# Performance work log

Hardware: AMD Instinct MI355X
Metric: run time of the kernel (lower is better)

Reference implementation:

```python
import jax, jax.numpy as jnp
import numpy as np

B, S, D = 8, 2048, 768


def setup_inputs() -> dict:
    key = jax.random.key(0)
    ks = jax.random.split(key, 16)
    def lin(kw, kb, din, dout):
        # torch nn.Linear default init: U(-1/sqrt(din), 1/sqrt(din))
        bound = 1.0 / np.sqrt(din)
        W = jax.random.uniform(kw, (din, dout), minval=-bound, maxval=bound, dtype=jnp.float32)
        b = jax.random.uniform(kb, (dout,), minval=-bound, maxval=bound, dtype=jnp.float32)
        return W, b
    Wq1, bq1 = lin(ks[0], ks[1], D, D)
    Wk1, bk1 = lin(ks[2], ks[3], D, D)
    Wv1, bv1 = lin(ks[4], ks[5], D, D)
    Wq2, bq2 = lin(ks[6], ks[7], D, D)
    Wk2, bk2 = lin(ks[8], ks[9], D, D)
    Wv2, bv2 = lin(ks[10], ks[11], D, D)
    Wf, bf = lin(ks[12], ks[13], 2 * D, D)
    self_x = jax.random.normal(ks[14], (B, S, D), dtype=jnp.float32)
    conv_x = jax.random.normal(ks[15], (B, S, D), dtype=jnp.float32)
    return {
        "self_x": self_x, "conv_x": conv_x,
        "Wq1": Wq1, "bq1": bq1, "Wk1": Wk1, "bk1": bk1, "Wv1": Wv1, "bv1": bv1,
        "Wq2": Wq2, "bq2": bq2, "Wk2": Wk2, "bk2": bk2, "Wv2": Wv2, "bv2": bv2,
        "Wf": Wf, "bf": bf,
    }


def reference(self_x, conv_x, Wq1, bq1, Wk1, bk1, Wv1, bv1,
              Wq2, bq2, Wk2, bk2, Wv2, bv2, Wf, bf):
    scale = jnp.asarray(Wk1.shape[-1] ** 0.5, dtype=self_x.dtype)

    # direction 1: queries from self_x, keys/values from conv_x
    Q1 = self_x @ Wq1 + bq1            # [B,S,D]
    K1 = conv_x @ Wk1 + bk1
    V1 = conv_x @ Wv1 + bv1
    attn1 = jnp.einsum('bqd,bkd->bqk', Q1, K1) / scale
    # NOTE: softmax over dim=1 (the QUERY axis), as in the original module
    w1 = jax.nn.softmax(attn1, axis=1)
    attn_out1 = jnp.einsum('bqk,bkd->bqd', w1, V1)

    # direction 2: queries from conv_x, keys/values from self_x
    Q2 = conv_x @ Wq2 + bq2
    K2 = self_x @ Wk2 + bk2
    V2 = self_x @ Wv2 + bv2
    attn2 = jnp.einsum('bqd,bkd->bqk', Q2, K2) / scale
    w2 = jax.nn.softmax(attn2, axis=1)
    attn_out2 = jnp.einsum('bqk,bkd->bqd', w2, V2)

    a1 = jax.nn.sigmoid(jnp.tanh(attn_out1))
    a2 = jax.nn.sigmoid(jnp.tanh(attn_out2))
    out1 = a2 * self_x + (1.0 - a2) * conv_x
    out2 = a1 * conv_x + (1.0 - a1) * self_x
    fused = jnp.concatenate([out1, out2], axis=-1)  # [B,S,2D]
    return fused @ Wf + bf
```

## Files before the change

kernel.cpp:

```cpp
#include <hip/hip_runtime.h>
#include <hip/hip_bf16.h>

#define BM 128
#define BN 128
#define BK 64

typedef short short8 __attribute__((ext_vector_type(8)));
typedef float f32x4 __attribute__((ext_vector_type(4)));

using bf = __hip_bfloat16;

static const int NOSPLIT = 1 << 30;

__device__ __forceinline__ void gld16(const void* g, void* l)
{
    __builtin_amdgcn_global_load_lds(
        (__attribute__((address_space(1))) void*)g,
        (__attribute__((address_space(3))) void*)l, 16, 0, 0);
}

__device__ __forceinline__ int lofs(int row, int kg8)
{
    return row * 64 + ((kg8 ^ (row & 7)) << 3);
}

__global__ __launch_bounds__(256)
void cast_bf16(const float* __restrict__ src, bf* __restrict__ dst, int n)
{
    int i = (blockIdx.x * 256 + threadIdx.x) * 4;
    if (i >= n) return;
    float4 v = *(const float4*)(src + i);
    bf o[4] = { __float2bfloat16(v.x), __float2bfloat16(v.y),
                __float2bfloat16(v.z), __float2bfloat16(v.w) };
    *(uint2*)(dst + i) = *(const uint2*)o;
}

__global__ __launch_bounds__(256)
void transpose_cast_w(const float* __restrict__ W, bf* __restrict__ Wt,
                      int Kd, int Nd)
{
    __shared__ float tile[32][33];
    int k0 = blockIdx.y * 32, n0 = blockIdx.x * 32;
    int t = threadIdx.x;
    int r = t >> 3, c = (t & 7) * 4;
    float4 v = *(const float4*)(W + (size_t)(k0 + r) * Nd + n0 + c);
    tile[r][c] = v.x; tile[r][c+1] = v.y; tile[r][c+2] = v.z; tile[r][c+3] = v.w;
    __syncthreads();
    bf o[4] = { __float2bfloat16(tile[c][r]),   __float2bfloat16(tile[c+1][r]),
                __float2bfloat16(tile[c+2][r]), __float2bfloat16(tile[c+3][r]) };
    *(uint2*)(Wt + (size_t)(n0 + r) * Kd + k0 + c) = *(const uint2*)o;
}

template <typename CT, bool TC>
__global__ __launch_bounds__(256)
void gemm_nt(const bf* __restrict__ A, const bf* __restrict__ A2, int splitA, int lda,
             const bf* __restrict__ Bt, int ldb,
             const float* __restrict__ bias, CT* __restrict__ C, int ldc,
             int K, long long strA, long long strB, long long strC)
{
    __shared__ __align__(16) ushort sA[2][BM * 64];
    __shared__ __align__(16) ushort sB[2][BN * 64];

    const int z = blockIdx.z;
    A  += (long long)z * strA;
    A2 += (long long)z * strA;
    Bt += (long long)z * strB;
    C  += (long long)z * strC;

    const int t = threadIdx.x;
    const int m0 = blockIdx.x * BM;
    const int n0 = blockIdx.y * BN;
    const int wave = t >> 6, lane = t & 63;
    const int wm = wave >> 1, wn = wave & 1;
    const int lcol = lane & 15, quad = lane >> 4;
    const int rl = lane >> 3, cslot = lane & 7;

    auto stage = [&](int kt, int c) {
        const bf* Asrc = (kt < splitA) ? A : A2;
        const int ktt = (kt < splitA) ? kt : kt - splitA;
        #pragma unroll
        for (int it = 0; it < 4; ++it) {
            int br  = it * 32 + wave * 8;
            int row = br + rl;
            int kg  = cslot ^ rl;
            gld16(Asrc + (size_t)(m0 + row) * lda + ktt + kg * 8, &sA[c][br * 64]);
            gld16(Bt   + (size_t)(n0 + row) * ldb + kt  + kg * 8, &sB[c][br * 64]);
        }
    };

    f32x4 acc[4][4] = {};

    stage(0, 0);
    __syncthreads();
    int cur = 0;
    for (int kt = 0; kt < K; kt += BK) {
        if (kt + BK < K) stage(kt + BK, cur ^ 1);

        #pragma unroll
        for (int h = 0; h < 2; ++h) {
            short8 af[4], bfr[4];
            #pragma unroll
            for (int i = 0; i < 4; ++i)
                af[i] = *(const short8*)&sA[cur][lofs(wm * 64 + i * 16 + lcol, h * 4 + quad)];
            #pragma unroll
            for (int j = 0; j < 4; ++j)
                bfr[j] = *(const short8*)&sB[cur][lofs(wn * 64 + j * 16 + lcol, h * 4 + quad)];
            #pragma unroll
            for (int i = 0; i < 4; ++i)
                #pragma unroll
                for (int j = 0; j < 4; ++j)
                    acc[i][j] = __builtin_amdgcn_mfma_f32_16x16x32_bf16(af[i], bfr[j], acc[i][j], 0, 0, 0);
        }
        __syncthreads();
        cur ^= 1;
    }

    #pragma unroll
    for (int j = 0; j < 4; ++j) {
        int col = n0 + wn * 64 + j * 16 + lcol;
        float bv = bias ? bias[col] : 0.0f;
        #pragma unroll
        for (int i = 0; i < 4; ++i) {
            int row = m0 + wm * 64 + i * 16 + quad * 4;
            if (!TC) {
                #pragma unroll
                for (int r4 = 0; r4 < 4; ++r4)
                    C[(size_t)(row + r4) * ldc + col] = (CT)(acc[i][j][r4] + bv);
            } else {
                bf o[4];
                #pragma unroll
                for (int r4 = 0; r4 < 4; ++r4)
                    o[r4] = __float2bfloat16(acc[i][j][r4] + bv);
                *(uint2*)((bf*)C + (size_t)col * ldc + row) = *(const uint2*)o;
            }
        }
    }
}

__global__ __launch_bounds__(256)
void scores_exp(const bf* __restrict__ Q, const bf* __restrict__ Km,
                bf* __restrict__ E, float* __restrict__ colsum,
                int Dd, float rscale)
{
    const int S = 2048;
    __shared__ __align__(16) ushort sA[2][BM * 64];
    __shared__ __align__(16) ushort sB[2][BN * 64];

    const int z = blockIdx.z;
    Q  += (size_t)z * S * Dd;
    Km += (size_t)z * S * Dd;
    E  += (size_t)z * S * S;
    colsum += (size_t)z * S;

    const int t = threadIdx.x;
    const int m0 = blockIdx.x * BM;
    const int n0 = blockIdx.y * BN;
    const int wave = t >> 6, lane = t & 63;
    const int wm = wave >> 1, wn = wave & 1;
    const int lcol = lane & 15, quad = lane >> 4;
    const int rl = lane >> 3, cslot = lane & 7;

    auto stage = [&](int kt, int c) {
        #pragma unroll
        for (int it = 0; it < 4; ++it) {
            int br  = it * 32 + wave * 8;
            int row = br + rl;
            int kg  = cslot ^ rl;
            gld16(Q  + (size_t)(m0 + row) * Dd + kt + kg * 8, &sA[c][br * 64]);
            gld16(Km + (size_t)(n0 + row) * Dd + kt + kg * 8, &sB[c][br * 64]);
        }
    };

    f32x4 acc[4][4] = {};

    stage(0, 0);
    __syncthreads();
    int cur = 0;
    for (int kt = 0; kt < Dd; kt += BK) {
        if (kt + BK < Dd) stage(kt + BK, cur ^ 1);

        #pragma unroll
        for (int h = 0; h < 2; ++h) {
            short8 af[4], bfr[4];
            #pragma unroll
            for (int i = 0; i < 4; ++i)
                af[i] = *(const short8*)&sA[cur][lofs(wm * 64 + i * 16 + lcol, h * 4 + quad)];
            #pragma unroll
            for (int j = 0; j < 4; ++j)
                bfr[j] = *(const short8*)&sB[cur][lofs(wn * 64 + j * 16 + lcol, h * 4 + quad)];
            #pragma unroll
            for (int a = 0; a < 4; ++a)
                #pragma unroll
                for (int b = 0; b < 4; ++b)
                    acc[a][b] = __builtin_amdgcn_mfma_f32_16x16x32_bf16(bfr[a], af[b], acc[a][b], 0, 0, 0);
        }
        __syncthreads();
        cur ^= 1;
    }

    #pragma unroll
    for (int a = 0; a < 4; ++a) {
        const int kk = n0 + wn * 64 + a * 16 + quad * 4;
        f32x4 csum = {0.f, 0.f, 0.f, 0.f};
        #pragma unroll
        for (int b = 0; b < 4; ++b) {
            const int q = m0 + wm * 64 + b * 16 + lcol;
            bf o[4];
            #pragma unroll
            for (int r = 0; r < 4; ++r) {
                float e = __expf(acc[a][b][r] * rscale);
                o[r] = __float2bfloat16(e);
                csum[r] += e;
            }
            *(uint2*)(E + (size_t)q * S + kk) = *(const uint2*)o;
        }
        #pragma unroll
        for (int msk = 1; msk < 16; msk <<= 1) {
            csum[0] += __shfl_xor(csum[0], msk);
            csum[1] += __shfl_xor(csum[1], msk);
            csum[2] += __shfl_xor(csum[2], msk);
            csum[3] += __shfl_xor(csum[3], msk);
        }
        if (lcol == 0) {
            atomicAdd(&colsum[kk + 0], csum[0]);
            atomicAdd(&colsum[kk + 1], csum[1]);
            atomicAdd(&colsum[kk + 2], csum[2]);
            atomicAdd(&colsum[kk + 3], csum[3]);
        }
    }
}

__global__ __launch_bounds__(256)
void scale_vt(bf* __restrict__ Vt, const float* __restrict__ cs, int ldv)
{
    int col = (blockIdx.x * 256 + threadIdx.x) * 4;
    bf* p = Vt + (size_t)blockIdx.y * ldv + col;
    bf v[4]; *(uint2*)v = *(const uint2*)p;
    float4 c4 = *(const float4*)(cs + col);
    v[0] = __float2bfloat16(__bfloat162float(v[0]) / c4.x);
    v[1] = __float2bfloat16(__bfloat162float(v[1]) / c4.y);
    v[2] = __float2bfloat16(__bfloat162float(v[2]) / c4.z);
    v[3] = __float2bfloat16(__bfloat162float(v[3]) / c4.w);
    *(uint2*)p = *(const uint2*)v;
}

__global__ __launch_bounds__(256)
void gate_fuse(const bf* __restrict__ O1, const bf* __restrict__ O2,
               const float* __restrict__ SX, const float* __restrict__ CX,
               bf* __restrict__ F1, bf* __restrict__ F2, int n)
{
    int i = (blockIdx.x * 256 + threadIdx.x) * 4;
    if (i >= n) return;
    bf o1[4], o2[4], f1[4], f2[4];
    *(uint2*)o1 = *(const uint2*)(O1 + i);
    *(uint2*)o2 = *(const uint2*)(O2 + i);
    float4 sx = *(const float4*)(SX + i);
    float4 cx = *(const float4*)(CX + i);
    #pragma unroll
    for (int e = 0; e < 4; ++e) {
        float s = (&sx.x)[e], c = (&cx.x)[e];
        float a1 = 1.0f / (1.0f + __expf(-tanhf(__bfloat162float(o1[e]))));
        float a2 = 1.0f / (1.0f + __expf(-tanhf(__bfloat162float(o2[e]))));
        f1[e] = __float2bfloat16(a2 * s + (1.0f - a2) * c);
        f2[e] = __float2bfloat16(a1 * c + (1.0f - a1) * s);
    }
    *(uint2*)(F1 + i) = *(const uint2*)f1;
    *(uint2*)(F2 + i) = *(const uint2*)f2;
}

extern "C" void kernel_launch(void* const* d_in, const int* in_sizes, int n_in,
                              void* d_out, int out_size, void* d_ws, size_t ws_size,
                              hipStream_t stream)
{
    const int B = 8, S = 2048, D = 768;
    const int M = B * S;

    const float* SX = (const float*)d_in[0];
    const float* CX = (const float*)d_in[1];
    const float* Wsrc[7] = { (const float*)d_in[2],  (const float*)d_in[4],
                             (const float*)d_in[6],  (const float*)d_in[8],
                             (const float*)d_in[10], (const float*)d_in[12],
                             (const float*)d_in[14] };
    const float* bias[7] = { (const float*)d_in[3],  (const float*)d_in[5],
                             (const float*)d_in[7],  (const float*)d_in[9],
                             (const float*)d_in[11], (const float*)d_in[13],
                             (const float*)d_in[15] };
    float* out = (float*)d_out;

    char* w = (char*)d_ws;
    const size_t MD  = (size_t)M * D * sizeof(bf);
    const size_t WSZ = (size_t)D * D * sizeof(bf);
    const size_t SSB = (size_t)S * S * sizeof(bf);
    bf* Xs = (bf*)(w);
    bf* Xc = (bf*)(w + MD);
    bf* Wt[7];
    for (int i = 0; i < 7; ++i) Wt[i] = (bf*)(w + 2 * MD + i * WSZ);
    char* base2 = w + 2 * MD + 8 * WSZ;
    bf* Q  = (bf*)(base2);
    bf* Kb = (bf*)(base2 + MD);
    bf* Vt = (bf*)(base2 + 2 * MD);
    bf* O1 = (bf*)(base2 + 3 * MD);
    float* cs = (float*)(base2 + 4 * MD);
    char* Eb0 = base2 + 4 * MD + (size_t)2 * B * S * sizeof(float);
    bf* E = (bf*)Eb0;
    int cb;
    {
        size_t fixed = (size_t)(Eb0 - w);
        size_t avail = ws_size > fixed ? ws_size - fixed : SSB;
        long long c = (long long)(avail / SSB);
        cb = c < 1 ? 1 : (c > 8 ? 8 : (int)c);
    }
    bf* O2 = Xs;
    bf* F1 = Kb;
    bf* F2 = Vt;

    (void)hipMemsetAsync(cs, 0, (size_t)2 * B * S * sizeof(float), stream);

    dim3 blk(256);
    {
        int n = M * D;
        cast_bf16<<<dim3(n / 1024), blk, 0, stream>>>(SX, Xs, n);
        cast_bf16<<<dim3(n / 1024), blk, 0, stream>>>(CX, Xc, n);
        for (int i = 0; i < 6; ++i)
            transpose_cast_w<<<dim3(D / 32, D / 32), blk, 0, stream>>>(Wsrc[i], Wt[i], D, D);
        transpose_cast_w<<<dim3(D / 32, 2 * D / 32), blk, 0, stream>>>(Wsrc[6], Wt[6], 2 * D, D);
    }

    dim3 gProj(M / BM, D / BN);
    const float rscale = 1.0f / sqrtf((float)D);
    const size_t SD = (size_t)S * D;
    const long long SS = (long long)S * S;

    for (int dir = 0; dir < 2; ++dir) {
        const bf* Xq = dir == 0 ? Xs : Xc;
        const bf* Xk = dir == 0 ? Xc : Xs;
        bf* Wq = Wt[dir * 3 + 0];
        bf* Wk = Wt[dir * 3 + 1];
        bf* Wv = Wt[dir * 3 + 2];
        const float* bq = bias[dir * 3 + 0];
        const float* bk = bias[dir * 3 + 1];
        const float* bv = bias[dir * 3 + 2];
        bf* O = dir == 0 ? O1 : O2;
        float* csd = cs + (size_t)dir * B * S;

        gemm_nt<bf, false><<<gProj, blk, 0, stream>>>(Xq, Xq, NOSPLIT, D, Wq, D, bq, Q,  D, D, 0, 0, 0);
        gemm_nt<bf, false><<<gProj, blk, 0, stream>>>(Xk, Xk, NOSPLIT, D, Wk, D, bk, Kb, D, D, 0, 0, 0);
        gemm_nt<bf, true ><<<gProj, blk, 0, stream>>>(Xk, Xk, NOSPLIT, D, Wv, D, bv, Vt, M, D, 0, 0, 0);

        for (int c0 = 0; c0 < B; c0 += cb) {
            int cbc = (B - c0 < cb) ? (B - c0) : cb;
            scores_exp<<<dim3(S / BM, S / BN, cbc), blk, 0, stream>>>(
                Q + c0 * SD, Kb + c0 * SD, E, csd + (size_t)c0 * S, D, rscale);
            scale_vt<<<dim3(cbc * S / 1024, D), blk, 0, stream>>>(
                Vt + (size_t)c0 * S, csd + (size_t)c0 * S, M);
            gemm_nt<bf, false><<<dim3(S / BM, D / BN, cbc), blk, 0, stream>>>(
                E, E, NOSPLIT, S, Vt + (size_t)c0 * S, M, nullptr,
                O + c0 * SD, D, S, SS, S, (long long)SD);
        }
    }

    gate_fuse<<<dim3(M * D / 1024), blk, 0, stream>>>(O1, O2, SX, CX, F1, F2, M * D);
    gemm_nt<float, false><<<gProj, blk, 0, stream>>>(F1, F2, D, D, Wt[6], 2 * D,
                                                     bias[6], out, D, 2 * D, 0, 0, 0);
}
```

Baseline: 842.8 us.

## Use 256x128 tiles with 512-thread blocks and BK=32 in GEMM kernels

Doubles the M tile to 256 rows and uses 8 waves (512 threads) per block, halving the K step to 32 with a new LDS swizzle and staging layout. The barrier moves to the top of the loop, so each iteration has one sync. The goal is more reuse of B tiles and better MFMA occupancy per CU. The cost is a shorter K step, which adds more barriers per K, and a launch bound of 512 threads with 4 blocks per CU, which may pressure registers.

```diff
diff --git a/kernel.cpp b/kernel.cpp
--- a/kernel.cpp
+++ b/kernel.cpp
@@ -1,9 +1,9 @@
 #include <hip/hip_runtime.h>
 #include <hip/hip_bf16.h>
 
-#define BM 128
+#define BM 256
 #define BN 128
-#define BK 64
+#define BK 32
 
 typedef short short8 __attribute__((ext_vector_type(8)));
 typedef float f32x4 __attribute__((ext_vector_type(4)));
@@ -21,7 +21,7 @@
 
 __device__ __forceinline__ int lofs(int row, int kg8)
 {
-    return row * 64 + ((kg8 ^ (row & 7)) << 3);
+    return row * 32 + ((kg8 ^ ((row >> 1) & 3)) << 3);
 }
 
 __global__ __launch_bounds__(256)
@@ -52,14 +52,14 @@
 }
 
 template <typename CT, bool TC>
-__global__ __launch_bounds__(256)
+__global__ __launch_bounds__(512, 4)
 void gemm_nt(const bf* __restrict__ A, const bf* __restrict__ A2, int splitA, int lda,
              const bf* __restrict__ Bt, int ldb,
              const float* __restrict__ bias, CT* __restrict__ C, int ldc,
              int K, long long strA, long long strB, long long strC)
 {
-    __shared__ __align__(16) ushort sA[2][BM * 64];
-    __shared__ __align__(16) ushort sB[2][BN * 64];
+    __shared__ __align__(16) ushort sA[2][BM * 32];
+    __shared__ __align__(16) ushort sB[2][BN * 32];
 
     const int z = blockIdx.z;
     A  += (long long)z * strA;
@@ -73,45 +73,43 @@
     const int wave = t >> 6, lane = t & 63;
     const int wm = wave >> 1, wn = wave & 1;
     const int lcol = lane & 15, quad = lane >> 4;
-    const int rl = lane >> 3, cslot = lane & 7;
+    const int rl = lane >> 2, cslot = lane & 3;
 
     auto stage = [&](int kt, int c) {
         const bf* Asrc = (kt < splitA) ? A : A2;
         const int ktt = (kt < splitA) ? kt : kt - splitA;
-        #pragma unroll
-        for (int it = 0; it < 4; ++it) {
-            int br  = it * 32 + wave * 8;
-            int row = br + rl;
-            int kg  = cslot ^ rl;
-            gld16(Asrc + (size_t)(m0 + row) * lda + ktt + kg * 8, &sA[c][br * 64]);
-            gld16(Bt   + (size_t)(n0 + row) * ldb + kt  + kg * 8, &sB[c][br * 64]);
+        const int kg = cslot ^ ((rl >> 1) & 3);
+        #pragma unroll
+        for (int it = 0; it < 2; ++it) {
+            int br = it * 128 + wave * 16;
+            gld16(Asrc + (size_t)(m0 + br + rl) * lda + ktt + kg * 8, &sA[c][br * 32]);
+        }
+        {
+            int br = wave * 16;
+            gld16(Bt + (size_t)(n0 + br + rl) * ldb + kt + kg * 8, &sB[c][br * 32]);
         }
     };
 
     f32x4 acc[4][4] = {};
 
     stage(0, 0);
-    __syncthreads();
     int cur = 0;
     for (int kt = 0; kt < K; kt += BK) {
+        __syncthreads();
         if (kt + BK < K) stage(kt + BK, cur ^ 1);
 
-        #pragma unroll
-        for (int h = 0; h < 2; ++h) {
-            short8 af[4], bfr[4];
-            #pragma unroll
-            for (int i = 0; i < 4; ++i)
-                af[i] = *(const short8*)&sA[cur][lofs(wm * 64 + i * 16 + lcol, h * 4 + quad)];
+        short8 af[4], bfr[4];
+        #pragma unroll
+        for (int i = 0; i < 4; ++i)
+            af[i] = *(const short8*)&sA[cur][lofs(wm * 64 + i * 16 + lcol, quad)];
+        #pragma unroll
+        for (int j = 0; j < 4; ++j)
+            bfr[j] = *(const short8*)&sB[cur][lofs(wn * 64 + j * 16 + lcol, quad)];
+        #pragma unroll
+        for (int i = 0; i < 4; ++i)
             #pragma unroll
             for (int j = 0; j < 4; ++j)
-                bfr[j] = *(const short8*)&sB[cur][lofs(wn * 64 + j * 16 + lcol, h * 4 + quad)];
-            #pragma unroll
-            for (int i = 0; i < 4; ++i)
-                #pragma unroll
-                for (int j = 0; j < 4; ++j)
-                    acc[i][j] = __builtin_amdgcn_mfma_f32_16x16x32_bf16(af[i], bfr[j], acc[i][j], 0, 0, 0);
-        }
-        __syncthreads();
+                acc[i][j] = __builtin_amdgcn_mfma_f32_16x16x32_bf16(af[i], bfr[j], acc[i][j], 0, 0, 0);
         cur ^= 1;
     }
 
@@ -137,14 +135,14 @@
     }
 }
 
-__global__ __launch_bounds__(256)
+__global__ __launch_bounds__(512, 4)
 void scores_exp(const bf* __restrict__ Q, const bf* __restrict__ Km,
                 bf* __restrict__ E, float* __restrict__ colsum,
                 int Dd, float rscale)
 {
     const int S = 2048;
-    __shared__ __align__(16) ushort sA[2][BM * 64];
-    __shared__ __align__(16) ushort sB[2][BN * 64];
+    __shared__ __align__(16) ushort sA[2][BM * 32];
+    __shared__ __align__(16) ushort sB[2][BN * 32];
 
     const int z = blockIdx.z;
     Q  += (size_t)z * S * Dd;
@@ -158,43 +156,41 @@
     const int wave = t >> 6, lane = t & 63;
     const int wm = wave >> 1, wn = wave & 1;
     const int lcol = lane & 15, quad = lane >> 4;
-    const int rl = lane >> 3, cslot = lane & 7;
+    const int rl = lane >> 2, cslot = lane & 3;
 
     auto stage = [&](int kt, int c) {
-        #pragma unroll
-        for (int it = 0; it < 4; ++it) {
-            int br  = it * 32 + wave * 8;
-            int row = br + rl;
-            int kg  = cslot ^ rl;
-            gld16(Q  + (size_t)(m0 + row) * Dd + kt + kg * 8, &sA[c][br * 64]);
-            gld16(Km + (size_t)(n0 + row) * Dd + kt + kg * 8, &sB[c][br * 64]);
+        const int kg = cslot ^ ((rl >> 1) & 3);
+        #pragma unroll
+        for (int it = 0; it < 2; ++it) {
+            int br = it * 128 + wave * 16;
+            gld16(Q + (size_t)(m0 + br + rl) * Dd + kt + kg * 8, &sA[c][br * 32]);
+        }
+        {
+            int br = wave * 16;
+            gld16(Km + (size_t)(n0 + br + rl) * Dd + kt + kg * 8, &sB[c][br * 32]);
         }
     };
 
     f32x4 acc[4][4] = {};
 
     stage(0, 0);
-    __syncthreads();
     int cur = 0;
     for (int kt = 0; kt < Dd; kt += BK) {
+        __syncthreads();
         if (kt + BK < Dd) stage(kt + BK, cur ^ 1);
 
-        #pragma unroll
-        for (int h = 0; h < 2; ++h) {
-            short8 af[4], bfr[4];
+        short8 af[4], bfr[4];
+        #pragma unroll
+        for (int i = 0; i < 4; ++i)
+            af[i] = *(const short8*)&sA[cur][lofs(wm * 64 + i * 16 + lcol, quad)];
+        #pragma unroll
+        for (int j = 0; j < 4; ++j)
+            bfr[j] = *(const short8*)&sB[cur][lofs(wn * 64 + j * 16 + lcol, quad)];
+        #pragma unroll
+        for (int a = 0; a < 4; ++a)
             #pragma unroll
-            for (int i = 0; i < 4; ++i)
-                af[i] = *(const short8*)&sA[cur][lofs(wm * 64 + i * 16 + lcol, h * 4 + quad)];
-            #pragma unroll
-            for (int j = 0; j < 4; ++j)
-                bfr[j] = *(const short8*)&sB[cur][lofs(wn * 64 + j * 16 + lcol, h * 4 + quad)];
-            #pragma unroll
-            for (int a = 0; a < 4; ++a)
-                #pragma unroll
-                for (int b = 0; b < 4; ++b)
-                    acc[a][b] = __builtin_amdgcn_mfma_f32_16x16x32_bf16(bfr[a], af[b], acc[a][b], 0, 0, 0);
-        }
-        __syncthreads();
+            for (int b = 0; b < 4; ++b)
+                acc[a][b] = __builtin_amdgcn_mfma_f32_16x16x32_bf16(bfr[a], af[b], acc[a][b], 0, 0, 0);
         cur ^= 1;
     }
 
@@ -317,6 +313,7 @@
     (void)hipMemsetAsync(cs, 0, (size_t)2 * B * S * sizeof(float), stream);
 
     dim3 blk(256);
+    dim3 blkG(512);
     {
         int n = M * D;
         cast_bf16<<<dim3(n / 1024), blk, 0, stream>>>(SX, Xs, n);
@@ -343,23 +340,23 @@
         bf* O = dir == 0 ? O1 : O2;
         float* csd = cs + (size_t)dir * B * S;
 
-        gemm_nt<bf, false><<<gProj, blk, 0, stream>>>(Xq, Xq, NOSPLIT, D, Wq, D, bq, Q,  D, D, 0, 0, 0);
-        gemm_nt<bf, false><<<gProj, blk, 0, stream>>>(Xk, Xk, NOSPLIT, D, Wk, D, bk, Kb, D, D, 0, 0, 0);
-        gemm_nt<bf, true ><<<gProj, blk, 0, stream>>>(Xk, Xk, NOSPLIT, D, Wv, D, bv, Vt, M, D, 0, 0, 0);
+        gemm_nt<bf, false><<<gProj, blkG, 0, stream>>>(Xq, Xq, NOSPLIT, D, Wq, D, bq, Q,  D, D, 0, 0, 0);
+        gemm_nt<bf, false><<<gProj, blkG, 0, stream>>>(Xk, Xk, NOSPLIT, D, Wk, D, bk, Kb, D, D, 0, 0, 0);
+        gemm_nt<bf, true ><<<gProj, blkG, 0, stream>>>(Xk, Xk, NOSPLIT, D, Wv, D, bv, Vt, M, D, 0, 0, 0);
 
         for (int c0 = 0; c0 < B; c0 += cb) {
             int cbc = (B - c0 < cb) ? (B - c0) : cb;
-            scores_exp<<<dim3(S / BM, S / BN, cbc), blk, 0, stream>>>(
+            scores_exp<<<dim3(S / BM, S / BN, cbc), blkG, 0, stream>>>(
                 Q + c0 * SD, Kb + c0 * SD, E, csd + (size_t)c0 * S, D, rscale);
             scale_vt<<<dim3(cbc * S / 1024, D), blk, 0, stream>>>(
                 Vt + (size_t)c0 * S, csd + (size_t)c0 * S, M);
-            gemm_nt<bf, false><<<dim3(S / BM, D / BN, cbc), blk, 0, stream>>>(
+            gemm_nt<bf, false><<<dim3(S / BM, D / BN, cbc), blkG, 0, stream>>>(
                 E, E, NOSPLIT, S, Vt + (size_t)c0 * S, M, nullptr,
                 O + c0 * SD, D, S, SS, S, (long long)SD);
         }
     }
 
     gate_fuse<<<dim3(M * D / 1024), blk, 0, stream>>>(O1, O2, SX, CX, F1, F2, M * D);
-    gemm_nt<float, false><<<gProj, blk, 0, stream>>>(F1, F2, D, D, Wt[6], 2 * D,
+    gemm_nt<float, false><<<gProj, blkG, 0, stream>>>(F1, F2, D, D, Wt[6], 2 * D,
                                                      bias[6], out, D, 2 * D, 0, 0, 0);
 }
```

After: 764.8 us. 9.3% less time.
